# Kernel optimization log

Measured on AMD Instinct MI355X. Metric: run time of the kernel, lower is better.

The kernel has to match this reference:

```python
import jax, jax.numpy as jnp
import numpy as np

NEG_BIG = 1e10


def setup_inputs() -> dict:
    key = jax.random.key(0)
    k1, k2 = jax.random.split(key)
    B, S, D = 8, 2048, 64
    T = 2048  # static tgt_max (stands in for tgt_lens.max())
    src_tok_features = jax.random.normal(k1, (B, S, D), dtype=jnp.float32)
    src_mask = jnp.ones((B, S), dtype=jnp.float32)
    lengthscale = jnp.array(1.0, dtype=jnp.float32)
    # lengths in [T//2, T] so tgt_lens != src_lens (skip identity branch) and no div-by-zero
    tgt_lens = jax.random.randint(k2, (B,), T // 2, T + 1, dtype=jnp.int32)
    return {
        "src_tok_features": src_tok_features,
        "src_mask": src_mask,
        "lengthscale": lengthscale,
        "tgt_lens": tgt_lens,
        "tgt_max": T,
    }


def reference(src_tok_features, src_mask, lengthscale, tgt_lens, tgt_max):
    # src_tok_features: (B, S, D); src_mask: (B, S) float; tgt_lens: (B,) int
    B, S, D = src_tok_features.shape
    T = int(tgt_max)
    src_lens = src_mask.sum(-1)                      # (B,)
    tl = tgt_lens.astype(src_lens.dtype)             # (B,)
    len_ratio = src_lens / tl                        # (B,)

    src_idx = jnp.arange(S, dtype=jnp.float32)       # (S,)
    tgt_idx = jnp.arange(T, dtype=jnp.float32)       # (T,)
    # (B, S, T): squared distance between src position and scaled tgt position
    sq_diff = (src_idx[None, :, None] - len_ratio[:, None, None] * tgt_idx[None, None, :]) ** 2
    logits = -sq_diff / (2.0 * lengthscale ** 2)
    m = src_mask[..., None]                          # (B, S, 1)
    logits = m * logits - (1.0 - m) * NEG_BIG
    weights = jax.nn.softmax(logits, axis=-2)        # normalize over src tokens
    # weighted sum over src dim without materializing (B, S, T, D)
    tgt_tok_features = jnp.einsum('bst,bsd->btd', weights, src_tok_features)
    tgt_mask = tgt_idx[None, :] < tl[:, None]        # (B, T) bool
    return tgt_tok_features, tgt_mask
```

## Files before the change

### kernel.cpp

```cpp
#include <hip/hip_runtime.h>
#include <hip/hip_bf16.h>

#ifndef NEG_BIG
#define NEG_BIG 1e10f
#endif

__global__ void prep_ratios(const float* __restrict__ mask,
                            const int* __restrict__ tgt_lens,
                            float* __restrict__ ratios, int S) {
    int b = blockIdx.x;
    float s = 0.f;
    for (int i = threadIdx.x; i < S; i += blockDim.x)
        s += mask[(size_t)b * S + i];
    for (int off = 32; off > 0; off >>= 1)
        s += __shfl_xor(s, off, 64);
    __shared__ float ws[8];
    int wid = threadIdx.x >> 6;
    int lane = threadIdx.x & 63;
    if (lane == 0) ws[wid] = s;
    __syncthreads();
    if (threadIdx.x == 0) {
        float tot = 0.f;
        int nw = blockDim.x >> 6;
        for (int i = 0; i < nw; i++) tot += ws[i];
        ratios[b] = tot / (float)tgt_lens[b];
    }
}

__global__ void __launch_bounds__(256)
length_transform(const float* __restrict__ x,
                 const float* __restrict__ mask,
                 const float* __restrict__ lengthscale,
                 const int* __restrict__ tgt_lens,
                 const float* __restrict__ ratios,
                 float* __restrict__ out_feat,
                 float* __restrict__ out_mask,
                 int B, int S, int T) {
    int gw = blockIdx.x * (blockDim.x >> 6) + (threadIdx.x >> 6);
    int lane = threadIdx.x & 63;
    if (gw >= B * T) return;
    int b = gw / T;
    int t = gw - b * T;

    float ls = lengthscale[0];
    float fac = 1.0f / (2.0f * ls * ls);
    float c = ratios[b] * (float)t;

    int s0 = (int)rintf(c) - 32;
    if (s0 < 0) s0 = 0;
    if (s0 > S - 64) s0 = S - 64;

    int s = s0 + lane;
    float ds = (float)s - c;
    float mv = mask[(size_t)b * S + s];
    float logit = mv * (-ds * ds * fac) - (1.0f - mv) * NEG_BIG;

    float mx = logit;
    for (int off = 32; off > 0; off >>= 1)
        mx = fmaxf(mx, __shfl_xor(mx, off, 64));
    float w = expf(logit - mx);
    float denom = w;
    for (int off = 32; off > 0; off >>= 1)
        denom += __shfl_xor(denom, off, 64);
    denom = fmaxf(denom, 1e-30f);
    float inv_denom = 1.0f / denom;

    const float* xrow = x + ((size_t)b * S + (size_t)s0) * 64 + lane;
    float acc = 0.f;
#pragma unroll 8
    for (int j = 0; j < 64; j++) {
        float wj = __shfl(w, j, 64);
        acc = fmaf(wj, xrow[(size_t)j * 64], acc);
    }

    out_feat[((size_t)b * T + t) * 64 + lane] = acc * inv_denom;
    if (lane == 0)
        out_mask[(size_t)b * T + t] = (t < tgt_lens[b]) ? 1.0f : 0.0f;
}

extern "C" void kernel_launch(void* const* d_in, const int* in_sizes, int n_in,
                              void* d_out, int out_size, void* d_ws, size_t ws_size,
                              hipStream_t stream) {
    const float* x        = (const float*)d_in[0];
    const float* mask     = (const float*)d_in[1];
    const float* ls       = (const float*)d_in[2];
    const int*   tgt_lens = (const int*)d_in[3];

    int B = in_sizes[3];
    int S = in_sizes[1] / B;
    int D = in_sizes[0] / (B * S);
    int T = out_size / (B * (D + 1));

    float* ratios = (float*)d_ws;
    float* out_feat = (float*)d_out;
    float* out_mask = out_feat + (size_t)B * T * D;

    prep_ratios<<<B, 256, 0, stream>>>(mask, tgt_lens, ratios, S);

    int waves = B * T;
    int wpb = 4;
    int grid = (waves + wpb - 1) / wpb;
    length_transform<<<grid, 256, 0, stream>>>(x, mask, ls, tgt_lens, ratios,
                                               out_feat, out_mask, B, S, T);
}
```

Measured before the change: 81.48 us.

## Process four target positions per wave sharing an 80-row source window

Each wave now handles four consecutive target positions. Their softmax weights are placed in LDS over a shared 80-row source window, and the feature rows are read once with float4 loads and reused across all four outputs, with partial sums combined by cross-lane shuffles. The max reduction is replaced by an analytic maximum taken at the nearest source index, which removes one shuffle reduction per target. The aim is to cut redundant global reads of x and per-target reduction overhead. In exchange it adds LDS traffic and block barriers, and it assumes T is divisible by 4 and that the four windows fit in 80 rows, which holds only when the length ratio is below about 5.

```diff
diff --git a/kernel.cpp b/kernel.cpp
--- a/kernel.cpp
+++ b/kernel.cpp
@@ -1,9 +1,7 @@
 #include <hip/hip_runtime.h>
 #include <hip/hip_bf16.h>
 
-#ifndef NEG_BIG
 #define NEG_BIG 1e10f
-#endif
 
 __global__ void prep_ratios(const float* __restrict__ mask,
                             const int* __restrict__ tgt_lens,
@@ -27,6 +25,9 @@
     }
 }
 
+constexpr int TPW = 4;
+constexpr int NROWS = 80;
+
 __global__ void __launch_bounds__(256)
 length_transform(const float* __restrict__ x,
                  const float* __restrict__ mask,
@@ -36,46 +37,102 @@
                  float* __restrict__ out_feat,
                  float* __restrict__ out_mask,
                  int B, int S, int T) {
-    int gw = blockIdx.x * (blockDim.x >> 6) + (threadIdx.x >> 6);
-    int lane = threadIdx.x & 63;
-    if (gw >= B * T) return;
-    int b = gw / T;
-    int t = gw - b * T;
+    __shared__ float4 wlds_all[4][NROWS];
+    const int wid  = threadIdx.x >> 6;
+    const int lane = threadIdx.x & 63;
+    const int nt = T / TPW;
+    int gw = blockIdx.x * 4 + wid;
+    const bool active = (gw < B * nt);
+    if (!active) gw = 0;
+    const int b  = gw / nt;
+    const int t0 = (gw - b * nt) * TPW;
 
-    float ls = lengthscale[0];
-    float fac = 1.0f / (2.0f * ls * ls);
-    float c = ratios[b] * (float)t;
+    const float ls = lengthscale[0];
+    const float fac = 1.0f / (2.0f * ls * ls);
+    const float r = ratios[b];
 
-    int s0 = (int)rintf(c) - 32;
-    if (s0 < 0) s0 = 0;
-    if (s0 > S - 64) s0 = S - 64;
-
-    int s = s0 + lane;
-    float ds = (float)s - c;
-    float mv = mask[(size_t)b * S + s];
-    float logit = mv * (-ds * ds * fac) - (1.0f - mv) * NEG_BIG;
-
-    float mx = logit;
-    for (int off = 32; off > 0; off >>= 1)
-        mx = fmaxf(mx, __shfl_xor(mx, off, 64));
-    float w = expf(logit - mx);
-    float denom = w;
-    for (int off = 32; off > 0; off >>= 1)
-        denom += __shfl_xor(denom, off, 64);
-    denom = fmaxf(denom, 1e-30f);
-    float inv_denom = 1.0f / denom;
-
-    const float* xrow = x + ((size_t)b * S + (size_t)s0) * 64 + lane;
-    float acc = 0.f;
-#pragma unroll 8
-    for (int j = 0; j < 64; j++) {
-        float wj = __shfl(w, j, 64);
-        acc = fmaf(wj, xrow[(size_t)j * 64], acc);
+    int su[TPW]; float c[TPW];
+#pragma unroll
+    for (int i = 0; i < TPW; ++i) {
+        c[i] = r * (float)(t0 + i);
+        int s0 = (int)rintf(c[i]) - 32;
+        if (s0 < 0) s0 = 0;
+        if (s0 > S - 64) s0 = S - 64;
+        su[i] = s0;
+    }
+    int u0 = su[0];
+    if (u0 > S - NROWS) u0 = S - NROWS;
+    if (u0 < 0) u0 = 0;
+#pragma unroll
+    for (int i = 0; i < TPW; ++i) {
+        int hi = u0 + (NROWS - 64);
+        su[i] = su[i] > hi ? hi : (su[i] < u0 ? u0 : su[i]);
     }
 
-    out_feat[((size_t)b * T + t) * 64 + lane] = acc * inv_denom;
-    if (lane == 0)
-        out_mask[(size_t)b * T + t] = (t < tgt_lens[b]) ? 1.0f : 0.0f;
+    float4* wlds = wlds_all[wid];
+    for (int i = lane; i < NROWS; i += 64)
+        wlds[i] = make_float4(0.f, 0.f, 0.f, 0.f);
+    __syncthreads();
+
+#pragma unroll
+    for (int i = 0; i < TPW; ++i) {
+        int s = su[i] + lane;
+        float dsv = (float)s - c[i];
+        float mv = mask[(size_t)b * S + s];
+        float logit = mv * (-dsv * dsv * fac) - (1.0f - mv) * NEG_BIG;
+        int sstar = (int)rintf(c[i]);
+        if (sstar < su[i]) sstar = su[i];
+        if (sstar > su[i] + 63) sstar = su[i] + 63;
+        float dstar = (float)sstar - c[i];
+        float mx = -dstar * dstar * fac;
+        float w = expf(logit - mx);
+        float dn = w;
+        for (int off = 32; off > 0; off >>= 1)
+            dn += __shfl_xor(dn, off, 64);
+        w *= 1.0f / fmaxf(dn, 1e-30f);
+        ((float*)&wlds[s - u0])[i] = w;
+    }
+    __syncthreads();
+
+    const int g = lane >> 4;
+    const int cidx = (lane & 15) << 2;
+    const float* xp = x + ((size_t)b * S + (size_t)(u0 + g)) * 64 + cidx;
+    float4 a0 = {0,0,0,0}, a1 = {0,0,0,0}, a2 = {0,0,0,0}, a3 = {0,0,0,0};
+#pragma unroll 5
+    for (int j = 0; j < NROWS / 4; ++j) {
+        float4 v  = *(const float4*)(xp + (size_t)(4 * j) * 64);
+        float4 wv = wlds[4 * j + g];
+        a0.x = fmaf(wv.x, v.x, a0.x); a0.y = fmaf(wv.x, v.y, a0.y);
+        a0.z = fmaf(wv.x, v.z, a0.z); a0.w = fmaf(wv.x, v.w, a0.w);
+        a1.x = fmaf(wv.y, v.x, a1.x); a1.y = fmaf(wv.y, v.y, a1.y);
+        a1.z = fmaf(wv.y, v.z, a1.z); a1.w = fmaf(wv.y, v.w, a1.w);
+        a2.x = fmaf(wv.z, v.x, a2.x); a2.y = fmaf(wv.z, v.y, a2.y);
+        a2.z = fmaf(wv.z, v.z, a2.z); a2.w = fmaf(wv.z, v.w, a2.w);
+        a3.x = fmaf(wv.w, v.x, a3.x); a3.y = fmaf(wv.w, v.y, a3.y);
+        a3.z = fmaf(wv.w, v.z, a3.z); a3.w = fmaf(wv.w, v.w, a3.w);
+    }
+
+#pragma unroll
+    for (int off = 16; off <= 32; off <<= 1) {
+        a0.x += __shfl_xor(a0.x, off, 64); a0.y += __shfl_xor(a0.y, off, 64);
+        a0.z += __shfl_xor(a0.z, off, 64); a0.w += __shfl_xor(a0.w, off, 64);
+        a1.x += __shfl_xor(a1.x, off, 64); a1.y += __shfl_xor(a1.y, off, 64);
+        a1.z += __shfl_xor(a1.z, off, 64); a1.w += __shfl_xor(a1.w, off, 64);
+        a2.x += __shfl_xor(a2.x, off, 64); a2.y += __shfl_xor(a2.y, off, 64);
+        a2.z += __shfl_xor(a2.z, off, 64); a2.w += __shfl_xor(a2.w, off, 64);
+        a3.x += __shfl_xor(a3.x, off, 64); a3.y += __shfl_xor(a3.y, off, 64);
+        a3.z += __shfl_xor(a3.z, off, 64); a3.w += __shfl_xor(a3.w, off, 64);
+    }
+
+    if (active) {
+        float4 myacc = a0;
+        if (g == 1) myacc = a1;
+        else if (g == 2) myacc = a2;
+        else if (g == 3) myacc = a3;
+        *(float4*)(out_feat + ((size_t)b * T + (size_t)(t0 + g)) * 64 + cidx) = myacc;
+        if (lane < TPW)
+            out_mask[(size_t)b * T + t0 + lane] = (t0 + lane < tgt_lens[b]) ? 1.0f : 0.0f;
+    }
 }
 
 extern "C" void kernel_launch(void* const* d_in, const int* in_sizes, int n_in,
@@ -97,9 +154,8 @@
 
     prep_ratios<<<B, 256, 0, stream>>>(mask, tgt_lens, ratios, S);
 
-    int waves = B * T;
-    int wpb = 4;
-    int grid = (waves + wpb - 1) / wpb;
+    int waves = B * (T / TPW);
+    int grid = (waves + 3) / 4;
     length_transform<<<grid, 256, 0, stream>>>(x, mask, ls, tgt_lens, ratios,
                                                out_feat, out_mask, B, S, T);
 }
```

Measured after the change: 72.71 us. 10.8% less time.
